# Performance work log

Hardware: AMD Instinct MI355X
Metric: run time of the kernel (lower is better)

## Reference

```python
import jax, jax.numpy as jnp
import numpy as np

# Lattice gauge L-CNN convolution (eq. 5 of arXiv:2012.12901), real-valued analogue.
B, L, D, KK, N_IN, N_OUT, NC = 2, 16, 4, 2, 8, 8, 3  # batch, side, dirs, kernel reach, channels, SU(3)


def setup_inputs() -> dict:
    key = jax.random.key(0)
    kW, kU, kO = jax.random.split(key, 3)
    # W: locally transforming variables, (batch, L1..L4, N_in, Nc, Nc)
    W = jax.random.normal(kW, (B, L, L, L, L, N_IN, NC, NC), dtype=jnp.float32)
    # U_PT: parallel transporters, (batch, L1..L4, d, 2K+1, Nc, Nc)
    U_PT = jax.random.normal(kU, (B, L, L, L, L, D, 2 * KK + 1, NC, NC), dtype=jnp.float32)
    # omega: conv coefficients, (N_out, N_in, d, 2K+1)
    omega = jax.random.normal(kO, (N_OUT, N_IN, D, 2 * KK + 1), dtype=jnp.float32) * 0.1
    return {"W": W, "U_PT": U_PT, "omega": omega}


def _apply_L_conv(W, U_PT, omega):
    """Gauge-equivariant lattice conv: shift + parallel-transport sandwich + accumulate.

    W:     (b, L1..Ld, N_in, Nc, Nc)
    U_PT:  (b, L1..Ld, d, 2K+1, Nc, Nc)
    omega: (N_out, N_in, d, 2K+1)
    returns (b, L1..Ld, N_out, Nc, Nc)
    """
    K = (U_PT.shape[-3] - 1) // 2
    d = U_PT.shape[-4]
    N_out = omega.shape[0]
    out = jnp.zeros(W.shape[:-3] + (N_out,) + W.shape[-2:], dtype=W.dtype)
    for k in range(-K, K + 1):          # fixed small kernel-offset loop
        i_k = k + K
        for mu in range(d):             # fixed small direction loop
            W_shift = jnp.roll(W, shift=-k, axis=1 + mu)
            U = U_PT[..., mu, i_k, :, :]  # (b, lattice, Nc, Nc)
            # torch: einsum('ij,...ac,...jcd,...db->...iab', om, U, Ws, U.adjoint())
            # real adjoint = transpose: (U^T)_{db} = U_{bd}
            out = out + jnp.einsum(
                'ij,...ac,...jcd,...bd->...iab',
                omega[..., mu, i_k], U, W_shift, U)
    return out


def reference(W, U_PT, omega):
    return _apply_L_conv(W, U_PT, omega)
```

## Files before the change

### kernel.cpp

```cpp
#include <hip/hip_runtime.h>

#define NSITES (2 * 16 * 16 * 16 * 16)

#define OM_MU_STRIDE 328

__global__ __launch_bounds__(256) void lconv_kernel(
    const float* __restrict__ W, const float* __restrict__ U_PT,
    const float* __restrict__ omega, float* __restrict__ out)
{
    __shared__ float s_om[4 * OM_MU_STRIDE];
    for (int t = threadIdx.x; t < 1280; t += 256) {
        const int i  = t / 160;
        const int r  = t - i * 160;
        const int j  = r / 20;
        const int r2 = r - j * 20;
        const int m  = r2 / 5;
        const int ik = r2 - m * 5;
        s_om[m * OM_MU_STRIDE + ik * 64 + j * 8 + i] = omega[t];
    }
    __syncthreads();

    const int bid = ((int)blockIdx.x & 7) * ((int)gridDim.x >> 3)
                  + ((int)blockIdx.x >> 3);
    const int idx = bid * 256 + (int)threadIdx.x;
    const int s   = idx >> 3;
    const int jh  = (idx >> 2) & 1;
    const int mu  = idx & 3;
    const int sh  = 12 - 4 * mu;
    const int x   = (s >> sh) & 15;

    const float* __restrict__ Ub  = U_PT + (size_t)s * 180 + mu * 45;
    const float* __restrict__ omt = s_om + mu * OM_MU_STRIDE + jh * 4;
    const int jown8 = jh * 32;
    const int jpar8 = (jh ^ 1) * 32;

    float acc[4][9];
#pragma unroll
    for (int i = 0; i < 4; ++i)
#pragma unroll
        for (int e = 0; e < 9; ++e) acc[i][e] = 0.0f;

#pragma unroll 1
    for (int ik = 0; ik < 5; ++ik) {
        const int k = ik - 2;
        float U[9];
#pragma unroll
        for (int e = 0; e < 9; ++e) U[e] = Ub[ik * 9 + e];

        const int ns = s + ((((x + k + 16) & 15) - x) << sh);
        const float4* __restrict__ Wn4 =
            reinterpret_cast<const float4*>(W + (size_t)ns * 72 + jh * 36);
        float Wl[36];
#pragma unroll
        for (int q = 0; q < 9; ++q) {
            const float4 v = Wn4[q];
            Wl[q * 4 + 0] = v.x; Wl[q * 4 + 1] = v.y;
            Wl[q * 4 + 2] = v.z; Wl[q * 4 + 3] = v.w;
        }

#pragma unroll
        for (int t = 0; t < 4; ++t) {
            float M[9];
#pragma unroll
            for (int a = 0; a < 3; ++a) {
                const float uw0 = fmaf(U[a * 3 + 0], Wl[t * 9 + 0],
                                  fmaf(U[a * 3 + 1], Wl[t * 9 + 3],
                                       U[a * 3 + 2] * Wl[t * 9 + 6]));
                const float uw1 = fmaf(U[a * 3 + 0], Wl[t * 9 + 1],
                                  fmaf(U[a * 3 + 1], Wl[t * 9 + 4],
                                       U[a * 3 + 2] * Wl[t * 9 + 7]));
                const float uw2 = fmaf(U[a * 3 + 0], Wl[t * 9 + 2],
                                  fmaf(U[a * 3 + 1], Wl[t * 9 + 5],
                                       U[a * 3 + 2] * Wl[t * 9 + 8]));
#pragma unroll
                for (int b2 = 0; b2 < 3; ++b2)
                    M[a * 3 + b2] = fmaf(uw0, U[b2 * 3 + 0],
                                    fmaf(uw1, U[b2 * 3 + 1],
                                         uw2 * U[b2 * 3 + 2]));
            }

            const float4 wo = *reinterpret_cast<const float4*>(
                                  omt + ik * 64 + jown8 + t * 8);
            const float4 wp = *reinterpret_cast<const float4*>(
                                  omt + ik * 64 + jpar8 + t * 8);
            const float wov[4] = {wo.x, wo.y, wo.z, wo.w};
            const float wpv[4] = {wp.x, wp.y, wp.z, wp.w};

#pragma unroll
            for (int e = 0; e < 9; ++e) {
                const float mp = __shfl_xor(M[e], 4);
#pragma unroll
                for (int ii = 0; ii < 4; ++ii)
                    acc[ii][e] = fmaf(wov[ii], M[e],
                                 fmaf(wpv[ii], mp, acc[ii][e]));
            }
        }
    }

#pragma unroll
    for (int i = 0; i < 4; ++i)
#pragma unroll
        for (int e = 0; e < 9; ++e) {
            float v = acc[i][e];
            v += __shfl_xor(v, 1);
            v += __shfl_xor(v, 2);
            acc[i][e] = v;
        }

    if (mu == 0) {
        float4* __restrict__ o4 =
            reinterpret_cast<float4*>(out + (size_t)s * 72 + jh * 36);
#pragma unroll
        for (int q = 0; q < 9; ++q) {
            const int f = q * 4;
            o4[q] = make_float4(acc[(f + 0) / 9][(f + 0) % 9],
                                acc[(f + 1) / 9][(f + 1) % 9],
                                acc[(f + 2) / 9][(f + 2) % 9],
                                acc[(f + 3) / 9][(f + 3) % 9]);
        }
    }
}

extern "C" void kernel_launch(void* const* d_in, const int* in_sizes, int n_in,
                              void* d_out, int out_size, void* d_ws, size_t ws_size,
                              hipStream_t stream) {
    const float* W   = (const float*)d_in[0];
    const float* U   = (const float*)d_in[1];
    const float* om  = (const float*)d_in[2];
    float*       out = (float*)d_out;

    const int block = 256;
    const int grid  = (NSITES * 8) / block;
    hipLaunchKernelGGL(lconv_kernel, dim3(grid), dim3(block), 0, stream,
                       W, U, om, out);
}
```

Before: 121.6 us.

## Software-pipeline W and U loads across kernel-offset iterations with register double buffering

The W tile for each shifted neighbour is now loaded in four 12-float chunks, each prefetched one step ahead into a two-slot register buffer. The next offset's U matrix is fetched before the current offset's compute runs. The aim is to hide global-load latency behind the FMA work, which the old code paid at the start of every ik iteration. In exchange, the live register count rises, which may lower occupancy or cause spills. The last iteration also issues redundant prefetch loads.

```diff
diff --git a/kernel.cpp b/kernel.cpp
--- a/kernel.cpp
+++ b/kernel.cpp
@@ -3,6 +3,24 @@
 #define NSITES (2 * 16 * 16 * 16 * 16)
 
 #define OM_MU_STRIDE 328
+
+__device__ __forceinline__ void loadU9(float* __restrict__ U,
+                                       const float* __restrict__ p) {
+#pragma unroll
+    for (int e = 0; e < 9; ++e) U[e] = p[e];
+}
+
+template <int T>
+__device__ __forceinline__ void loadWch(float* __restrict__ dst,
+                                        const float4* __restrict__ base) {
+    constexpr int q0 = (T * 9) >> 2;
+#pragma unroll
+    for (int q = 0; q < 3; ++q) {
+        const float4 v = base[q0 + q];
+        dst[q * 4 + 0] = v.x; dst[q * 4 + 1] = v.y;
+        dst[q * 4 + 2] = v.z; dst[q * 4 + 3] = v.w;
+    }
+}
 
 __global__ __launch_bounds__(256) void lconv_kernel(
     const float* __restrict__ W, const float* __restrict__ U_PT,
@@ -40,38 +58,45 @@
 #pragma unroll
         for (int e = 0; e < 9; ++e) acc[i][e] = 0.0f;
 
+    const float4* Wp_c = reinterpret_cast<const float4*>(
+        W + (size_t)(s + ((((x - 2 + 16) & 15) - x) << sh)) * 72 + jh * 36);
+    float Wf[2][12];
+    loadWch<0>(Wf[0], Wp_c);
+    float U[9];
+    loadU9(U, Ub);
+
 #pragma unroll 1
     for (int ik = 0; ik < 5; ++ik) {
-        const int k = ik - 2;
-        float U[9];
-#pragma unroll
-        for (int e = 0; e < 9; ++e) U[e] = Ub[ik * 9 + e];
-
-        const int ns = s + ((((x + k + 16) & 15) - x) << sh);
-        const float4* __restrict__ Wn4 =
-            reinterpret_cast<const float4*>(W + (size_t)ns * 72 + jh * 36);
-        float Wl[36];
-#pragma unroll
-        for (int q = 0; q < 9; ++q) {
-            const float4 v = Wn4[q];
-            Wl[q * 4 + 0] = v.x; Wl[q * 4 + 1] = v.y;
-            Wl[q * 4 + 2] = v.z; Wl[q * 4 + 3] = v.w;
-        }
+        const int ikn = (ik < 4) ? ik + 1 : ik;
+        const int kn  = ikn - 2;
+        const float4* Wp_n = reinterpret_cast<const float4*>(
+            W + (size_t)(s + ((((x + kn + 16) & 15) - x) << sh)) * 72 + jh * 36);
+        float Un[9];
+        loadU9(Un, Ub + ikn * 9);
 
 #pragma unroll
         for (int t = 0; t < 4; ++t) {
+            const int p   = t & 1;
+            const int off = (t * 9) & 3;
+            if (t == 0)      loadWch<1>(Wf[p ^ 1], Wp_c);
+            else if (t == 1) loadWch<2>(Wf[p ^ 1], Wp_c);
+            else if (t == 2) loadWch<3>(Wf[p ^ 1], Wp_c);
+            else             loadWch<0>(Wf[p ^ 1], Wp_n);
+
+            const float* __restrict__ Wc = Wf[p] + off;
+
             float M[9];
 #pragma unroll
             for (int a = 0; a < 3; ++a) {
-                const float uw0 = fmaf(U[a * 3 + 0], Wl[t * 9 + 0],
-                                  fmaf(U[a * 3 + 1], Wl[t * 9 + 3],
-                                       U[a * 3 + 2] * Wl[t * 9 + 6]));
-                const float uw1 = fmaf(U[a * 3 + 0], Wl[t * 9 + 1],
-                                  fmaf(U[a * 3 + 1], Wl[t * 9 + 4],
-                                       U[a * 3 + 2] * Wl[t * 9 + 7]));
-                const float uw2 = fmaf(U[a * 3 + 0], Wl[t * 9 + 2],
-                                  fmaf(U[a * 3 + 1], Wl[t * 9 + 5],
-                                       U[a * 3 + 2] * Wl[t * 9 + 8]));
+                const float uw0 = fmaf(U[a * 3 + 0], Wc[0],
+                                  fmaf(U[a * 3 + 1], Wc[3],
+                                       U[a * 3 + 2] * Wc[6]));
+                const float uw1 = fmaf(U[a * 3 + 0], Wc[1],
+                                  fmaf(U[a * 3 + 1], Wc[4],
+                                       U[a * 3 + 2] * Wc[7]));
+                const float uw2 = fmaf(U[a * 3 + 0], Wc[2],
+                                  fmaf(U[a * 3 + 1], Wc[5],
+                                       U[a * 3 + 2] * Wc[8]));
 #pragma unroll
                 for (int b2 = 0; b2 < 3; ++b2)
                     M[a * 3 + b2] = fmaf(uw0, U[b2 * 3 + 0],
@@ -95,6 +120,10 @@
                                  fmaf(wpv[ii], mp, acc[ii][e]));
             }
         }
+
+        Wp_c = Wp_n;
+#pragma unroll
+        for (int e = 0; e < 9; ++e) U[e] = Un[e];
     }
 
 #pragma unroll
```

After: 164.2 us. 35.0% more time.

## Stage shifted W neighbor tiles in LDS per block and prefetch U

Applied to the files above, without the earlier changes.

Each block of 32 sites now cooperatively loads its central W tile and, for each nonzero shift, the three shifted neighbor tiles for directions 0-2 into LDS with coalesced float4 loads. Direction 3 shifts stay within the 32-site row, so they read the central tile. Threads then read W from LDS instead of issuing scattered global loads, and the next U matrix is prefetched one step ahead. This adds two barriers per offset and about 44KB of LDS per block, which can lower occupancy.

```diff
diff --git a/kernel.cpp b/kernel.cpp
--- a/kernel.cpp
+++ b/kernel.cpp
@@ -2,35 +2,69 @@
 
 #define NSITES (2 * 16 * 16 * 16 * 16)
 
-#define OM_MU_STRIDE 328
+#define OM_OFF     0
+#define CENT_OFF   1316
+#define REG_OFF    3752
+#define REG_STRIDE 2436
+#define SITE_F     76
+#define LDS_FLOATS (REG_OFF + 3 * REG_STRIDE)
+
+__device__ __forceinline__ void loadU9(float* __restrict__ U,
+                                       const float* __restrict__ p) {
+#pragma unroll
+    for (int e = 0; e < 9; ++e) U[e] = p[e];
+}
 
 __global__ __launch_bounds__(256) void lconv_kernel(
     const float* __restrict__ W, const float* __restrict__ U_PT,
     const float* __restrict__ omega, float* __restrict__ out)
 {
-    __shared__ float s_om[4 * OM_MU_STRIDE];
-    for (int t = threadIdx.x; t < 1280; t += 256) {
+    __shared__ float lds[LDS_FLOATS];
+    const int tid = threadIdx.x;
+
+    for (int t = tid; t < 1280; t += 256) {
         const int i  = t / 160;
         const int r  = t - i * 160;
         const int j  = r / 20;
         const int r2 = r - j * 20;
         const int m  = r2 / 5;
         const int ik = r2 - m * 5;
-        s_om[m * OM_MU_STRIDE + ik * 64 + j * 8 + i] = omega[t];
-    }
-    __syncthreads();
+        lds[OM_OFF + m * 328 + ik * 64 + j * 8 + i] = omega[t];
+    }
 
     const int bid = ((int)blockIdx.x & 7) * ((int)gridDim.x >> 3)
                   + ((int)blockIdx.x >> 3);
-    const int idx = bid * 256 + (int)threadIdx.x;
-    const int s   = idx >> 3;
-    const int jh  = (idx >> 2) & 1;
-    const int mu  = idx & 3;
-    const int sh  = 12 - 4 * mu;
-    const int x   = (s >> sh) & 15;
+    const int s0  = bid * 32;
+
+    {
+        const float4* __restrict__ W4 =
+            reinterpret_cast<const float4*>(W) + (size_t)s0 * 18;
+#pragma unroll
+        for (int q = 0; q < 3; ++q) {
+            const int flat = q * 256 + tid;
+            if (flat < 576) {
+                const int lsite = flat / 18;
+                const int f4    = flat - lsite * 18;
+                *reinterpret_cast<float4*>(
+                    lds + CENT_OFF + lsite * SITE_F + f4 * 4) =
+                    W4[lsite * 18 + f4];
+            }
+        }
+    }
+
+    const int local = tid >> 3;
+    const int s     = s0 + local;
+    const int jh    = (tid >> 2) & 1;
+    const int mu    = tid & 3;
+    const int x3    = s & 15;
+    const int x2b   = (s >> 4) & 1;
+
+    const int c0 = (s0 >> 12) & 15;
+    const int c1 = (s0 >> 8) & 15;
+    const int c2 = (s0 >> 4) & 15;
 
     const float* __restrict__ Ub  = U_PT + (size_t)s * 180 + mu * 45;
-    const float* __restrict__ omt = s_om + mu * OM_MU_STRIDE + jh * 4;
+    const float* __restrict__ omt = lds + OM_OFF + mu * 328 + jh * 4;
     const int jown8 = jh * 32;
     const int jpar8 = (jh ^ 1) * 32;
 
@@ -40,20 +74,54 @@
 #pragma unroll
         for (int e = 0; e < 9; ++e) acc[i][e] = 0.0f;
 
+    float U[9];
+    loadU9(U, Ub);
+
 #pragma unroll 1
     for (int ik = 0; ik < 5; ++ik) {
-        const int k = ik - 2;
-        float U[9];
-#pragma unroll
-        for (int e = 0; e < 9; ++e) U[e] = Ub[ik * 9 + e];
-
-        const int ns = s + ((((x + k + 16) & 15) - x) << sh);
-        const float4* __restrict__ Wn4 =
-            reinterpret_cast<const float4*>(W + (size_t)ns * 72 + jh * 36);
+        const int k   = ik - 2;
+        const int ikn = (ik < 4) ? ik + 1 : ik;
+        float Un[9];
+        loadU9(Un, Ub + ikn * 9);
+
+        if (k != 0) {
+            const int d0  = ((((c0 + k) & 15) - c0) << 12);
+            const int d1  = ((((c1 + k) & 15) - c1) << 8);
+            const int d2a = ((((c2 + k) & 15) - c2) << 4);
+            const int d2b = ((((c2 + 1 + k) & 15) - (c2 + 1)) << 4);
+            const float4* __restrict__ W4 =
+                reinterpret_cast<const float4*>(W);
+#pragma unroll
+            for (int q = 0; q < 7; ++q) {
+                const int flat = q * 256 + tid;
+                if (flat < 1728) {
+                    const int r     = flat / 576;
+                    const int rem   = flat - r * 576;
+                    const int lsite = rem / 18;
+                    const int f4    = rem - lsite * 18;
+                    const int delta = (r == 0) ? d0
+                                    : (r == 1) ? d1
+                                    : ((lsite >= 16) ? d2b : d2a);
+                    *reinterpret_cast<float4*>(
+                        lds + REG_OFF + r * REG_STRIDE
+                            + lsite * SITE_F + f4 * 4) =
+                        W4[(size_t)(s0 + lsite + delta) * 18 + f4];
+                }
+            }
+        }
+        __syncthreads();
+
+        const int  use_cent = (k == 0) || (mu == 3);
+        const float* __restrict__ wbase =
+            use_cent ? (lds + CENT_OFF) : (lds + REG_OFF + mu * REG_STRIDE);
+        const int lb = (mu == 3 && k != 0)
+                     ? (((x3 + k) & 15) + x2b * 16) : local;
+        const float* __restrict__ Wp = wbase + lb * SITE_F + jh * 36;
+
         float Wl[36];
 #pragma unroll
         for (int q = 0; q < 9; ++q) {
-            const float4 v = Wn4[q];
+            const float4 v = *reinterpret_cast<const float4*>(Wp + q * 4);
             Wl[q * 4 + 0] = v.x; Wl[q * 4 + 1] = v.y;
             Wl[q * 4 + 2] = v.z; Wl[q * 4 + 3] = v.w;
         }
@@ -95,6 +163,10 @@
                                  fmaf(wpv[ii], mp, acc[ii][e]));
             }
         }
+        __syncthreads();
+
+#pragma unroll
+        for (int e = 0; e < 9; ++e) U[e] = Un[e];
     }
 
 #pragma unroll
@@ -130,7 +202,7 @@
     float*       out = (float*)d_out;
 
     const int block = 256;
-    const int grid  = (NSITES * 8) / block;
+    const int grid  = NSITES / 32;
     hipLaunchKernelGGL(lconv_kernel, dim3(grid), dim3(block), 0, stream,
                        W, U, om, out);
 }
```

Result: slower. 142.8 us (+17.4%).

## Stage U_PT and block-local W sites in LDS with coalesced float4 loads

Applied to the files above, without the earlier changes.

Each block now cooperatively loads its 32 sites' U_PT transporters and W values into shared memory with coalesced float4 loads, then reads U from LDS. For the unshifted offset and for shifts along the fastest lattice axis (mu==3), the neighbour W is read from the staged LDS tile instead of global memory; the other shifts still read global. This targets the uncoalesced strided per-thread global loads of U and part of the W traffic, at the cost of more LDS use (lower occupancy) and a divergent branch between LDS and global paths within a wavefront.

```diff
diff --git a/kernel.cpp b/kernel.cpp
--- a/kernel.cpp
+++ b/kernel.cpp
@@ -2,35 +2,71 @@
 
 #define NSITES (2 * 16 * 16 * 16 * 16)
 
-#define OM_MU_STRIDE 328
+#define OM_OFF 0
+#define U_OFF  1312
+#define C_OFF  (1312 + 5888)
+#define LDS_FLOATS (C_OFF + 2432)
 
 __global__ __launch_bounds__(256) void lconv_kernel(
     const float* __restrict__ W, const float* __restrict__ U_PT,
     const float* __restrict__ omega, float* __restrict__ out)
 {
-    __shared__ float s_om[4 * OM_MU_STRIDE];
-    for (int t = threadIdx.x; t < 1280; t += 256) {
-        const int i  = t / 160;
-        const int r  = t - i * 160;
-        const int j  = r / 20;
-        const int r2 = r - j * 20;
-        const int m  = r2 / 5;
-        const int ik = r2 - m * 5;
-        s_om[m * OM_MU_STRIDE + ik * 64 + j * 8 + i] = omega[t];
+    __shared__ float lds[LDS_FLOATS];
+    const int tid = threadIdx.x;
+
+    const int bid = ((int)blockIdx.x & 7) * ((int)gridDim.x >> 3)
+                  + ((int)blockIdx.x >> 3);
+    const int s0  = bid * 32;
+
+    {
+        const int site = tid >> 3;
+        const int r8   = tid & 7;
+
+        for (int t = tid; t < 1280; t += 256) {
+            const int i  = t / 160;
+            const int r  = t - i * 160;
+            const int j  = r / 20;
+            const int r2 = r - j * 20;
+            const int m  = r2 / 5;
+            const int ik = r2 - m * 5;
+            lds[OM_OFF + m * 328 + ik * 64 + j * 8 + i] = omega[t];
+        }
+
+        const float4* __restrict__ U4 =
+            reinterpret_cast<const float4*>(U_PT) + (size_t)s0 * 45;
+#pragma unroll
+        for (int st = 0; st < 6; ++st) {
+            const int f4r = st * 8 + r8;
+            if (st < 5 || f4r < 45) {
+                *reinterpret_cast<float4*>(
+                    lds + U_OFF + site * 184 + f4r * 4) =
+                    U4[site * 45 + f4r];
+            }
+        }
+
+        const float4* __restrict__ W4 =
+            reinterpret_cast<const float4*>(W) + (size_t)s0 * 18;
+#pragma unroll
+        for (int st = 0; st < 3; ++st) {
+            const int f4r = st * 8 + r8;
+            if (st < 2 || f4r < 18) {
+                *reinterpret_cast<float4*>(
+                    lds + C_OFF + site * 76 + f4r * 4) =
+                    W4[site * 18 + f4r];
+            }
+        }
     }
     __syncthreads();
 
-    const int bid = ((int)blockIdx.x & 7) * ((int)gridDim.x >> 3)
-                  + ((int)blockIdx.x >> 3);
-    const int idx = bid * 256 + (int)threadIdx.x;
-    const int s   = idx >> 3;
-    const int jh  = (idx >> 2) & 1;
-    const int mu  = idx & 3;
-    const int sh  = 12 - 4 * mu;
-    const int x   = (s >> sh) & 15;
+    const int local = tid >> 3;
+    const int s     = s0 + local;
+    const int jh    = (tid >> 2) & 1;
+    const int mu    = tid & 3;
+    const int sh    = 12 - 4 * mu;
+    const int x     = (s >> sh) & 15;
 
-    const float* __restrict__ Ub  = U_PT + (size_t)s * 180 + mu * 45;
-    const float* __restrict__ omt = s_om + mu * OM_MU_STRIDE + jh * 4;
+    const float* __restrict__ Ul  = lds + U_OFF + local * 184 + mu * 45;
+    const float* __restrict__ omt = lds + OM_OFF + mu * 328 + jh * 4;
     const int jown8 = jh * 32;
     const int jpar8 = (jh ^ 1) * 32;
 
@@ -43,19 +79,34 @@
 #pragma unroll 1
     for (int ik = 0; ik < 5; ++ik) {
         const int k = ik - 2;
+
         float U[9];
 #pragma unroll
-        for (int e = 0; e < 9; ++e) U[e] = Ub[ik * 9 + e];
+        for (int e = 0; e < 9; ++e) U[e] = Ul[ik * 9 + e];
 
-        const int ns = s + ((((x + k + 16) & 15) - x) << sh);
-        const float4* __restrict__ Wn4 =
-            reinterpret_cast<const float4*>(W + (size_t)ns * 72 + jh * 36);
+        const int  lbw     = ((local + k) & 15) | (local & 16);
+        const bool use_lds = (k == 0) || (mu == 3);
+
         float Wl[36];
+        if (use_lds) {
+            const float4* __restrict__ Wp = reinterpret_cast<const float4*>(
+                lds + C_OFF + lbw * 76 + jh * 36);
 #pragma unroll
-        for (int q = 0; q < 9; ++q) {
-            const float4 v = Wn4[q];
-            Wl[q * 4 + 0] = v.x; Wl[q * 4 + 1] = v.y;
-            Wl[q * 4 + 2] = v.z; Wl[q * 4 + 3] = v.w;
+            for (int q = 0; q < 9; ++q) {
+                const float4 v = Wp[q];
+                Wl[q * 4 + 0] = v.x; Wl[q * 4 + 1] = v.y;
+                Wl[q * 4 + 2] = v.z; Wl[q * 4 + 3] = v.w;
+            }
+        } else {
+            const int ns = s + ((((x + k + 16) & 15) - x) << sh);
+            const float4* __restrict__ Wp = reinterpret_cast<const float4*>(
+                W + (size_t)ns * 72 + jh * 36);
+#pragma unroll
+            for (int q = 0; q < 9; ++q) {
+                const float4 v = Wp[q];
+                Wl[q * 4 + 0] = v.x; Wl[q * 4 + 1] = v.y;
+                Wl[q * 4 + 2] = v.z; Wl[q * 4 + 3] = v.w;
+            }
         }
 
 #pragma unroll
@@ -130,7 +181,7 @@
     float*       out = (float*)d_out;
 
     const int block = 256;
-    const int grid  = (NSITES * 8) / block;
+    const int grid  = NSITES / 32;
     hipLaunchKernelGGL(lconv_kernel, dim3(grid), dim3(block), 0, stream,
                        W, U, om, out);
 }
```

Result: faster. 111.7 us (-8.2%).
